# Optimization experiments

Measured on AMD Instinct MI355X. Metric: run time of the kernel, lower is better.

Reference implementation:

```python
import jax, jax.numpy as jnp
import numpy as np

SIGMA_D = 1.0
SCALES = (0.1, 0.2, 0.4)
K_VALUES = (5, 10, 25)  # defaults of get_knn_indices
HIDDEN = 64


def _safe_sqrt(x):
    # sqrt with a tiny floor so diagonal zeros don't produce nan grads;
    # fwd diff vs exact sqrt is <= 1e-6 (only on the zero diagonal).
    return jnp.sqrt(jnp.where(x > 0, x, 1e-12))


def _l2norm(x, eps=1e-12):
    # F.normalize(dim=-1)
    n = jnp.linalg.norm(x, axis=-1, keepdims=True)
    return x / jnp.maximum(n, eps)


def setup_inputs() -> dict:
    key = jax.random.key(0)
    ks = jax.random.split(key, 7)
    B, N = 1, 1024
    S = len(SCALES)
    points = jax.random.normal(ks[0], (B, N, 3), dtype=jnp.float32)
    # torch Linear weights stored as (in, out): y = x @ W + b
    W_rtdie = jax.random.normal(ks[1], (1, HIDDEN), dtype=jnp.float32)
    b_rtdie = jax.random.normal(ks[2], (HIDDEN,), dtype=jnp.float32) * 0.01
    W_mdve = jax.random.normal(ks[3], (2 * S, HIDDEN), dtype=jnp.float32) / np.sqrt(2 * S)
    b_mdve = jax.random.normal(ks[4], (HIDDEN,), dtype=jnp.float32) * 0.01
    W_lgee = jax.random.normal(ks[5], (S, HIDDEN), dtype=jnp.float32) / np.sqrt(S)
    b_lgee = jax.random.normal(ks[6], (HIDDEN,), dtype=jnp.float32) * 0.01
    return {"points": points, "W_rtdie": W_rtdie, "b_rtdie": b_rtdie,
            "W_mdve": W_mdve, "b_mdve": b_mdve, "W_lgee": W_lgee, "b_lgee": b_lgee}


def reference(points, W_rtdie, b_rtdie, W_mdve, b_mdve, W_lgee, b_lgee):
    B, N, _ = points.shape
    # single pairwise distance map reused by every branch (torch recomputes it)
    diff = points[:, :, None, :] - points[:, None, :, :]      # (B,N,N,3)
    d2 = jnp.sum(diff * diff, axis=-1)                         # (B,N,N)
    dist = _safe_sqrt(d2)

    # rtdie: exp(-dist/sigma_d) -> Linear(1,H); computed under no_grad in torch
    # and only sets the output broadcast shape — it does NOT enter the output.

    # mdve: multi-scale density + density-gradient
    scales = jnp.asarray(SCALES, dtype=points.dtype)           # (S,)
    vols = (4.0 / 3.0) * np.pi * scales ** 3                   # (S,)
    within = (dist[..., None] < scales).astype(points.dtype)   # (B,N,N,S)
    density = jnp.sum(within, axis=2) / vols                   # (B,N,S)
    dd = density[:, :, None, :] - density[:, None, :, :]       # (B,N,N,S)
    gradient = _safe_sqrt(jnp.sum(dd * dd, axis=2))            # (B,N,S)
    mdve = _l2norm(jnp.concatenate([density, gradient], axis=-1))  # (B,N,2S)

    # lgee: kNN-distance entropy at multiple k
    ents = []
    for k in K_VALUES:
        kk = min(k, N - 1)
        nd = -jax.lax.top_k(-dist, kk + 1)[0][..., 1:]         # (B,N,k) smallest, drop self
        p = nd / jnp.sum(nd, axis=-1, keepdims=True)
        ents.append(-jnp.sum(p * jnp.log(p + 1e-10), axis=-1))
    lgee = _l2norm(jnp.stack(ents, axis=-1))                   # (B,N,len(K))

    mdve_e = _l2norm(mdve @ W_mdve + b_mdve)                   # (B,N,H)
    lgee_e = _l2norm(lgee @ W_lgee + b_lgee)                   # (B,N,H)
    s = mdve_e + lgee_e
    # expand_as(r_d_embeddings): out[0,i,j,h] = s[0,j,h]  (requires B==1)
    return jnp.broadcast_to(s[:, None, :, :], (B, N, N, HIDDEN))
```

## Files before the change

kernel.cpp:

```cpp
#include <hip/hip_runtime.h>
#include <math.h>

#define NPTS 1024
#define HID 64

typedef float v4f __attribute__((ext_vector_type(4)));

__global__ __launch_bounds__(64) void k_rows(const float* __restrict__ pts,
                                             float* __restrict__ density,
                                             float* __restrict__ ent,
                                             unsigned int* __restrict__ icnt) {
    const int i    = blockIdx.x;
    const int lane = threadIdx.x;

    const float px = pts[i * 3 + 0];
    const float py = pts[i * 3 + 1];
    const float pz = pts[i * 3 + 2];

    float v[16];
    int c0 = 0, c1 = 0, c2 = 0;
    #pragma unroll
    for (int q = 0; q < 16; ++q) {
        const int j = lane + q * 64;
        float dx = __fsub_rn(px, pts[j * 3 + 0]);
        float dy = __fsub_rn(py, pts[j * 3 + 1]);
        float dz = __fsub_rn(pz, pts[j * 3 + 2]);
        float d2 = __fadd_rn(__fadd_rn(__fmul_rn(dx, dx), __fmul_rn(dy, dy)),
                             __fmul_rn(dz, dz));
        float d = __fsqrt_rn(d2 > 0.0f ? d2 : 1e-12f);
        v[q] = d;
        c0 += (d < 0.1f);
        c1 += (d < 0.2f);
        c2 += (d < 0.4f);
    }

    unsigned long long packed = (unsigned long long)c0
                              | ((unsigned long long)c1 << 21)
                              | ((unsigned long long)c2 << 42);
    #pragma unroll
    for (int off = 32; off > 0; off >>= 1) packed += __shfl_xor(packed, off);

    #pragma unroll
    for (int k = 2; k <= 16; k <<= 1) {
        #pragma unroll
        for (int j = k >> 1; j > 0; j >>= 1) {
            #pragma unroll
            for (int r = 0; r < 16; ++r) {
                const int l = r ^ j;
                if (l > r) {
                    const bool up = ((r & k) == 0);
                    float lo = fminf(v[r], v[l]);
                    float hi = fmaxf(v[r], v[l]);
                    v[r] = up ? lo : hi;
                    v[l] = up ? hi : lo;
                }
            }
        }
    }

    float s[32];
    #pragma unroll
    for (int r = 0; r < 16; ++r) { s[r] = v[r]; s[16 + r] = 3.0e38f; }

    #pragma unroll
    for (int step = 1; step < 64; step <<= 1) {
        float o[32];
        #pragma unroll
        for (int r = 0; r < 32; ++r) o[r] = __shfl_xor(s[r], step);
        float m[32];
        #pragma unroll
        for (int r = 0; r < 32; ++r) m[r] = fminf(s[r], o[31 - r]);
        #pragma unroll
        for (int j = 16; j > 0; j >>= 1) {
            #pragma unroll
            for (int r = 0; r < 32; ++r) {
                const int l = r ^ j;
                if (l > r) {
                    float lo = fminf(m[r], m[l]);
                    float hi = fmaxf(m[r], m[l]);
                    m[r] = lo;
                    m[l] = hi;
                }
            }
        }
        #pragma unroll
        for (int r = 0; r < 32; ++r) s[r] = m[r];
    }

    const int kvv[3] = {5, 10, 25};
    float E[3];
    #pragma unroll
    for (int q = 0; q < 3; ++q) {
        const int k = kvv[q];
        float S = 0.0f;
        #pragma unroll
        for (int r = 1; r <= 25; ++r) if (r <= k) S += s[r];
        float Ee = 0.0f;
        #pragma unroll
        for (int r = 1; r <= 25; ++r) if (r <= k) {
            float p = s[r] / S;
            Ee -= p * logf(p + 1e-10f);
        }
        E[q] = Ee;
    }

    if (lane == 0) {
        ent[i * 3 + 0] = E[0];
        ent[i * 3 + 1] = E[1];
        ent[i * 3 + 2] = E[2];
        const float scl[3] = {0.1f, 0.2f, 0.4f};
        unsigned int cc[3] = {(unsigned int)(packed & 0x1FFFFF),
                              (unsigned int)((packed >> 21) & 0x1FFFFF),
                              (unsigned int)(packed >> 42)};
        #pragma unroll
        for (int s2 = 0; s2 < 3; ++s2) {
            float sv  = scl[s2];
            float vol = __fmul_rn((float)(4.0 / 3.0 * M_PI),
                                  __fmul_rn(__fmul_rn(sv, sv), sv));
            density[i * 3 + s2] = (float)cc[s2] / vol;
            icnt[i * 3 + s2] = cc[s2];
        }
    }
}

__global__ __launch_bounds__(256) void k_bcast(const float* __restrict__ density,
                                               const float* __restrict__ ent,
                                               const unsigned int* __restrict__ icnt,
                                               const float* __restrict__ Wm,
                                               const float* __restrict__ bm,
                                               const float* __restrict__ Wl,
                                               const float* __restrict__ bl,
                                               v4f* __restrict__ out) {
    __shared__ float  s_lds[16 * HID];
    __shared__ double sS[6];
    const int b    = blockIdx.x;
    const int c    = b & 63;
    const int g    = b >> 6;
    const int t    = threadIdx.x;
    const int lane = t & 63;
    const int w    = t >> 6;

    if (w == 0) {
        unsigned int sa0 = 0, sa1 = 0, sa2 = 0, sb0 = 0, sb1 = 0, sb2 = 0;
        #pragma unroll
        for (int r = 0; r < 16; ++r) {
            const int row = lane * 16 + r;
            unsigned int c0 = icnt[row * 3 + 0];
            unsigned int c1 = icnt[row * 3 + 1];
            unsigned int c2 = icnt[row * 3 + 2];
            sa0 += c0; sa1 += c1; sa2 += c2;
            sb0 += c0 * c0; sb1 += c1 * c1; sb2 += c2 * c2;
        }
        #pragma unroll
        for (int off = 32; off > 0; off >>= 1) {
            sa0 += __shfl_xor(sa0, off); sa1 += __shfl_xor(sa1, off);
            sa2 += __shfl_xor(sa2, off); sb0 += __shfl_xor(sb0, off);
            sb1 += __shfl_xor(sb1, off); sb2 += __shfl_xor(sb2, off);
        }
        if (lane == 0) {
            const float scl[3] = {0.1f, 0.2f, 0.4f};
            unsigned int A[3] = {sa0, sa1, sa2};
            unsigned int B[3] = {sb0, sb1, sb2};
            #pragma unroll
            for (int s = 0; s < 3; ++s) {
                float sv   = scl[s];
                float volf = __fmul_rn((float)(4.0 / 3.0 * M_PI),
                                       __fmul_rn(__fmul_rn(sv, sv), sv));
                double vold = (double)volf;
                sS[s]     = (double)A[s] / vold;
                sS[3 + s] = (double)B[s] / (vold * vold);
            }
        }
    }
    __syncthreads();

    double S1[3], S2[3];
    #pragma unroll
    for (int s = 0; s < 3; ++s) { S1[s] = sS[s]; S2[s] = sS[3 + s]; }

    #pragma unroll
    for (int kk = 0; kk < 4; ++kk) {
        const int row = 16 * c + 4 * w + kk;

        float m6[6];
        double nrm6 = 0.0;
        #pragma unroll
        for (int s = 0; s < 3; ++s) {
            float d = density[row * 3 + s];
            m6[s] = d;
            double dd = (double)d;
            double g2 = 1024.0 * dd * dd - 2.0 * dd * S1[s] + S2[s];
            m6[3 + s] = (float)sqrt(g2 > 0.0 ? g2 : 1e-12);
        }
        #pragma unroll
        for (int s = 0; s < 6; ++s) nrm6 += (double)m6[s] * (double)m6[s];
        float inv6 = 1.0f / fmaxf((float)sqrt(nrm6), 1e-12f);
        #pragma unroll
        for (int s = 0; s < 6; ++s) m6[s] *= inv6;

        float l3[3];
        double nrm3 = 0.0;
        #pragma unroll
        for (int s = 0; s < 3; ++s) {
            l3[s] = ent[row * 3 + s];
            nrm3 += (double)l3[s] * (double)l3[s];
        }
        float inv3 = 1.0f / fmaxf((float)sqrt(nrm3), 1e-12f);
        #pragma unroll
        for (int s = 0; s < 3; ++s) l3[s] *= inv3;

        float y = bm[lane];
        #pragma unroll
        for (int s = 0; s < 6; ++s) y += m6[s] * Wm[s * HID + lane];
        float yy = y * y;
        #pragma unroll
        for (int off = 32; off > 0; off >>= 1) yy += __shfl_xor(yy, off);
        y *= 1.0f / fmaxf(sqrtf(yy), 1e-12f);

        float z = bl[lane];
        #pragma unroll
        for (int s = 0; s < 3; ++s) z += l3[s] * Wl[s * HID + lane];
        float zz = z * z;
        #pragma unroll
        for (int off = 32; off > 0; off >>= 1) zz += __shfl_xor(zz, off);
        z *= 1.0f / fmaxf(sqrtf(zz), 1e-12f);

        s_lds[(4 * w + kk) * HID + lane] = y + z;
    }
    __syncthreads();

    const v4f val = *(const v4f*)&s_lds[4 * t];

    v4f* dst = out + (size_t)(g * 32) * (NPTS * HID / 4) + c * 256 + t;
    #pragma unroll 4
    for (int ii = 0; ii < 32; ++ii) {
        *dst = val;
        dst += NPTS * HID / 4;
    }
}

extern "C" void kernel_launch(void* const* d_in, const int* in_sizes, int n_in,
                              void* d_out, int out_size, void* d_ws, size_t ws_size,
                              hipStream_t stream) {
    const float* pts = (const float*)d_in[0];
    const float* Wm = (const float*)d_in[3];
    const float* bm = (const float*)d_in[4];
    const float* Wl = (const float*)d_in[5];
    const float* bl = (const float*)d_in[6];

    char* ws = (char*)d_ws;
    float*        density = (float*)(ws);
    float*        entv    = (float*)(ws + 12288);
    unsigned int* icnt    = (unsigned int*)(ws + 24576);

    float* out = (float*)d_out;

    hipLaunchKernelGGL(k_rows, dim3(NPTS), dim3(64), 0, stream,
                       pts, density, entv, icnt);
    hipLaunchKernelGGL(k_bcast, dim3(64 * 32), dim3(256), 0, stream,
                       density, entv, icnt, Wm, bm, Wl, bl, (v4f*)out);
}
```

Baseline: 68.47 us.

## Split per-row kNN selection across four wavefronts with shared-memory merge

```diff
diff --git a/kernel.cpp b/kernel.cpp
--- a/kernel.cpp
+++ b/kernel.cpp
@@ -6,22 +6,50 @@
 
 typedef float v4f __attribute__((ext_vector_type(4)));
 
-__global__ __launch_bounds__(64) void k_rows(const float* __restrict__ pts,
-                                             float* __restrict__ density,
-                                             float* __restrict__ ent,
-                                             unsigned int* __restrict__ icnt) {
+#define MERGE32(S, O)                                            \
+    do {                                                         \
+        float _m[32];                                            \
+        _Pragma("unroll")                                        \
+        for (int _r = 0; _r < 32; ++_r)                          \
+            _m[_r] = fminf((S)[_r], (O)[31 - _r]);               \
+        _Pragma("unroll")                                        \
+        for (int _j = 16; _j > 0; _j >>= 1) {                    \
+            _Pragma("unroll")                                    \
+            for (int _r = 0; _r < 32; ++_r) {                    \
+                const int _l = _r ^ _j;                          \
+                if (_l > _r) {                                   \
+                    float _lo = fminf(_m[_r], _m[_l]);           \
+                    float _hi = fmaxf(_m[_r], _m[_l]);           \
+                    _m[_r] = _lo;                                \
+                    _m[_l] = _hi;                                \
+                }                                                \
+            }                                                    \
+        }                                                        \
+        _Pragma("unroll")                                        \
+        for (int _r = 0; _r < 32; ++_r) (S)[_r] = _m[_r];        \
+    } while (0)
+
+__global__ __launch_bounds__(256) void k_rows(const float* __restrict__ pts,
+                                              float* __restrict__ density,
+                                              float* __restrict__ ent,
+                                              unsigned int* __restrict__ icnt) {
+    __shared__ float s_arr[4][32];
+    __shared__ unsigned long long s_cnt[4];
+
     const int i    = blockIdx.x;
-    const int lane = threadIdx.x;
+    const int t    = threadIdx.x;
+    const int lane = t & 63;
+    const int w    = t >> 6;
 
     const float px = pts[i * 3 + 0];
     const float py = pts[i * 3 + 1];
     const float pz = pts[i * 3 + 2];
 
-    float v[16];
+    float v[4];
     int c0 = 0, c1 = 0, c2 = 0;
     #pragma unroll
-    for (int q = 0; q < 16; ++q) {
-        const int j = lane + q * 64;
+    for (int q = 0; q < 4; ++q) {
+        const int j = w * 256 + q * 64 + lane;
         float dx = __fsub_rn(px, pts[j * 3 + 0]);
         float dy = __fsub_rn(py, pts[j * 3 + 1]);
         float dz = __fsub_rn(pz, pts[j * 3 + 2]);
@@ -39,86 +67,78 @@
                               | ((unsigned long long)c2 << 42);
     #pragma unroll
     for (int off = 32; off > 0; off >>= 1) packed += __shfl_xor(packed, off);
-
-    #pragma unroll
-    for (int k = 2; k <= 16; k <<= 1) {
-        #pragma unroll
-        for (int j = k >> 1; j > 0; j >>= 1) {
-            #pragma unroll
-            for (int r = 0; r < 16; ++r) {
-                const int l = r ^ j;
-                if (l > r) {
-                    const bool up = ((r & k) == 0);
-                    float lo = fminf(v[r], v[l]);
-                    float hi = fmaxf(v[r], v[l]);
-                    v[r] = up ? lo : hi;
-                    v[l] = up ? hi : lo;
-                }
-            }
-        }
+    if (lane == 0) s_cnt[w] = packed;
+
+    {
+        float lo, hi;
+        lo = fminf(v[0], v[1]); hi = fmaxf(v[0], v[1]); v[0] = lo; v[1] = hi;
+        lo = fminf(v[2], v[3]); hi = fmaxf(v[2], v[3]); v[2] = lo; v[3] = hi;
+        lo = fminf(v[0], v[2]); hi = fmaxf(v[0], v[2]); v[0] = lo; v[2] = hi;
+        lo = fminf(v[1], v[3]); hi = fmaxf(v[1], v[3]); v[1] = lo; v[3] = hi;
+        lo = fminf(v[1], v[2]); hi = fmaxf(v[1], v[2]); v[1] = lo; v[2] = hi;
     }
 
     float s[32];
     #pragma unroll
-    for (int r = 0; r < 16; ++r) { s[r] = v[r]; s[16 + r] = 3.0e38f; }
+    for (int r = 0; r < 32; ++r) s[r] = (r < 4) ? v[r] : 3.0e38f;
 
     #pragma unroll
     for (int step = 1; step < 64; step <<= 1) {
         float o[32];
         #pragma unroll
         for (int r = 0; r < 32; ++r) o[r] = __shfl_xor(s[r], step);
-        float m[32];
-        #pragma unroll
-        for (int r = 0; r < 32; ++r) m[r] = fminf(s[r], o[31 - r]);
-        #pragma unroll
-        for (int j = 16; j > 0; j >>= 1) {
-            #pragma unroll
-            for (int r = 0; r < 32; ++r) {
-                const int l = r ^ j;
-                if (l > r) {
-                    float lo = fminf(m[r], m[l]);
-                    float hi = fmaxf(m[r], m[l]);
-                    m[r] = lo;
-                    m[l] = hi;
-                }
+        MERGE32(s, o);
+    }
+
+    if (lane < 32) s_arr[w][lane] = s[lane];
+    __syncthreads();
+
+    if (w == 0) {
+        float o[32];
+        #pragma unroll
+        for (int r = 0; r < 32; ++r) o[r] = s_arr[1][r];
+        MERGE32(s, o);
+        #pragma unroll
+        for (int r = 0; r < 32; ++r) o[r] = s_arr[2][r];
+        MERGE32(s, o);
+        #pragma unroll
+        for (int r = 0; r < 32; ++r) o[r] = s_arr[3][r];
+        MERGE32(s, o);
+
+        const int kvv[3] = {5, 10, 25};
+        float E[3];
+        #pragma unroll
+        for (int q = 0; q < 3; ++q) {
+            const int k = kvv[q];
+            float S = 0.0f;
+            #pragma unroll
+            for (int r = 1; r <= 25; ++r) if (r <= k) S += s[r];
+            float Ee = 0.0f;
+            #pragma unroll
+            for (int r = 1; r <= 25; ++r) if (r <= k) {
+                float p = s[r] / S;
+                Ee -= p * logf(p + 1e-10f);
             }
-        }
-        #pragma unroll
-        for (int r = 0; r < 32; ++r) s[r] = m[r];
-    }
-
-    const int kvv[3] = {5, 10, 25};
-    float E[3];
-    #pragma unroll
-    for (int q = 0; q < 3; ++q) {
-        const int k = kvv[q];
-        float S = 0.0f;
-        #pragma unroll
-        for (int r = 1; r <= 25; ++r) if (r <= k) S += s[r];
-        float Ee = 0.0f;
-        #pragma unroll
-        for (int r = 1; r <= 25; ++r) if (r <= k) {
-            float p = s[r] / S;
-            Ee -= p * logf(p + 1e-10f);
-        }
-        E[q] = Ee;
-    }
-
-    if (lane == 0) {
-        ent[i * 3 + 0] = E[0];
-        ent[i * 3 + 1] = E[1];
-        ent[i * 3 + 2] = E[2];
-        const float scl[3] = {0.1f, 0.2f, 0.4f};
-        unsigned int cc[3] = {(unsigned int)(packed & 0x1FFFFF),
-                              (unsigned int)((packed >> 21) & 0x1FFFFF),
-                              (unsigned int)(packed >> 42)};
-        #pragma unroll
-        for (int s2 = 0; s2 < 3; ++s2) {
-            float sv  = scl[s2];
-            float vol = __fmul_rn((float)(4.0 / 3.0 * M_PI),
-                                  __fmul_rn(__fmul_rn(sv, sv), sv));
-            density[i * 3 + s2] = (float)cc[s2] / vol;
-            icnt[i * 3 + s2] = cc[s2];
+            E[q] = Ee;
+        }
+
+        if (lane == 0) {
+            unsigned long long ptot = s_cnt[0] + s_cnt[1] + s_cnt[2] + s_cnt[3];
+            ent[i * 3 + 0] = E[0];
+            ent[i * 3 + 1] = E[1];
+            ent[i * 3 + 2] = E[2];
+            const float scl[3] = {0.1f, 0.2f, 0.4f};
+            unsigned int cc[3] = {(unsigned int)(ptot & 0x1FFFFF),
+                                  (unsigned int)((ptot >> 21) & 0x1FFFFF),
+                                  (unsigned int)(ptot >> 42)};
+            #pragma unroll
+            for (int s2 = 0; s2 < 3; ++s2) {
+                float sv  = scl[s2];
+                float vol = __fmul_rn((float)(4.0 / 3.0 * M_PI),
+                                      __fmul_rn(__fmul_rn(sv, sv), sv));
+                density[i * 3 + s2] = (float)cc[s2] / vol;
+                icnt[i * 3 + s2] = cc[s2];
+            }
         }
     }
 }
@@ -255,7 +275,7 @@
 
     float* out = (float*)d_out;
 
-    hipLaunchKernelGGL(k_rows, dim3(NPTS), dim3(64), 0, stream,
+    hipLaunchKernelGGL(k_rows, dim3(NPTS), dim3(256), 0, stream,
                        pts, density, entv, icnt);
     hipLaunchKernelGGL(k_bcast, dim3(64 * 32), dim3(256), 0, stream,
                        density, entv, icnt, Wm, bm, Wl, bl, (v4f*)out);
```

New measurement: 72.23 us. +5.5%, slower.
